# Optimization experiments

Measured on AMD Instinct MI355X. Metric: run time of the kernel, lower is better.

Reference implementation:

```python
import jax, jax.numpy as jnp
import numpy as np


def setup_inputs() -> dict:
    key = jax.random.key(0)
    ks = jax.random.split(key, 8)
    B, H, W, D, U = 128, 16, 48, 512, 512
    s = 1.0 / np.sqrt(D)
    return {
        "dec_hidden": jax.random.normal(ks[0], (B, D), jnp.float32),
        "enc_output": jax.random.normal(ks[1], (B, H, W, D), jnp.float32),
        "W1_w": jax.random.normal(ks[2], (D, U), jnp.float32) * s,
        "W1_b": jnp.zeros((U,), jnp.float32),
        "W2_w": jax.random.normal(ks[3], (D, U), jnp.float32) * s,
        "W2_b": jnp.zeros((U,), jnp.float32),
        "V_w": jax.random.normal(ks[4], (U, 1), jnp.float32) * (1.0 / np.sqrt(U)),
        "V_b": jnp.zeros((1,), jnp.float32),
    }


def reference(dec_hidden, enc_output, W1_w, W1_b, W2_w, W2_b, V_w, V_b):
    # dec_hidden: [B, Dd] -> [B, 1, 1, Dd]
    dec = dec_hidden[:, None, None, :]
    # W1(enc_output): [B, H, W, U]; W2(dec): [B, 1, 1, U] (broadcast add)
    h = jnp.tanh(jnp.einsum('bhwd,du->bhwu', enc_output, W1_w) + W1_b
                 + (dec @ W2_w + W2_b))
    # V(.) -> score [B, H, W, 1]
    score = jnp.einsum('bhwu,uo->bhwo', h, V_w) + V_b
    # softmax over axis=1 (H axis), matching tf.keras softmax(score, axis=1)
    attention_weights = jax.nn.softmax(score, axis=1)
    # context: sum over spatial axes -> [B, D]
    context_vector = jnp.sum(attention_weights * enc_output, axis=(1, 2))
    return context_vector, attention_weights
```

## Files before the change

### kernel.cpp

```cpp
#include <hip/hip_runtime.h>
#include <hip/hip_bf16.h>

typedef __attribute__((ext_vector_type(8))) short short8;
typedef __attribute__((ext_vector_type(4))) float f32x4;
typedef unsigned short ushort;

#define BB 128
#define HHH 16
#define WWW 48
#define DD 512
#define UU 512
#define ROWS_PER_B (HHH * WWW)
#define MTOT (BB * ROWS_PER_B)

__device__ __forceinline__ ushort f2bf(float f) {
    unsigned int u = __float_as_uint(f);
    u += 0x7fffu + ((u >> 16) & 1u);
    return (ushort)(u >> 16);
}

__device__ __forceinline__ void gload_lds16(const ushort* g, ushort* l) {
    __builtin_amdgcn_global_load_lds(
        (const __attribute__((address_space(1))) unsigned int*)(const void*)g,
        (__attribute__((address_space(3))) unsigned int*)(void*)l,
        16, 0, 0);
}

__global__ __launch_bounds__(256) void prep_kernel(
        const float* __restrict__ w1, const float* __restrict__ dec,
        const float* __restrict__ w2, const float* __restrict__ w1b,
        const float* __restrict__ w2b,
        ushort* __restrict__ w1p, float* __restrict__ dproj) {
    const int t = threadIdx.x;
    if (blockIdx.x < 64) {
        __shared__ __align__(16) ushort tile[64 * 72];
        const int u0 = (blockIdx.x & 7) * 64;
        const int kc = blockIdx.x >> 3;
        const int ul = t & 63;
        const int db = t >> 6;
#pragma unroll
        for (int i = 0; i < 16; ++i) {
            const int d = db + i * 4;
            tile[ul * 72 + d] = f2bf(w1[(size_t)(kc * 64 + d) * UU + u0 + ul]);
        }
        __syncthreads();
        const int u = t >> 2;
        const int s = (t & 3) * 2;
        const int x = u & 7;
        short8 v0 = *(const short8*)&tile[u * 72 + s * 8];
        short8 v1 = *(const short8*)&tile[u * 72 + s * 8 + 8];
        *(short8*)&w1p[(size_t)kc * 32768 + (u0 + u) * 64 + (( s      ^ x)) * 8] = v0;
        *(short8*)&w1p[(size_t)kc * 32768 + (u0 + u) * 64 + (((s + 1) ^ x)) * 8] = v1;
    } else {
        const int g = blockIdx.x - 64;
        const int b = g >> 1;
        const int u = (g & 1) * 256 + t;
        float acc = 0.f;
#pragma unroll 8
        for (int d = 0; d < DD; ++d)
            acc += dec[b * DD + d] * w2[(size_t)d * UU + u];
        dproj[b * UU + u] = acc + w1b[u] + w2b[u];
    }
}

__global__ __launch_bounds__(512, 2) void score_kernel(
        const float* __restrict__ enc, const ushort* __restrict__ w1p,
        const float* __restrict__ dproj, const float* __restrict__ vw,
        const float* __restrict__ vb, float* __restrict__ score) {
    __shared__ __align__(16) ushort Bb[2][UU * 64];
    __shared__ __align__(16) ushort Ab[2][128 * 64];

    const int tid  = threadIdx.x;
    const int lane = tid & 63;
    const int wave = tid >> 6;
    const int mbase = blockIdx.x * 128;
    const int b = mbase / ROWS_PER_B;

    const int mh   = wave >> 2;
    const int uc   = wave & 3;
    const int lrow = lane & 15;
    const int kgrp = lane >> 4;

    const int ar  = tid >> 2;
    const int asp = (tid & 3) * 2;
    const float* abase = enc + (size_t)(mbase + ar) * DD + asp * 8;
    const int s0p = ( asp      ^ (ar & 7)) * 8;
    const int s1p = ((asp + 1) ^ (ar & 7)) * 8;

    f32x4 acc[4][8] = {};

    {
        float4 a0 = ((const float4*)abase)[0];
        float4 a1 = ((const float4*)abase)[1];
        float4 a2 = ((const float4*)abase)[2];
        float4 a3 = ((const float4*)abase)[3];
        const ushort* bsrc = w1p + tid * 8;
#pragma unroll
        for (int i = 0; i < 8; ++i)
            gload_lds16(bsrc + i * 4096, &Bb[0][tid * 8 + i * 4096]);
        short8 w0, w1v;
        ushort* p0 = (ushort*)&w0; ushort* p1 = (ushort*)&w1v;
        p0[0]=f2bf(a0.x); p0[1]=f2bf(a0.y); p0[2]=f2bf(a0.z); p0[3]=f2bf(a0.w);
        p0[4]=f2bf(a1.x); p0[5]=f2bf(a1.y); p0[6]=f2bf(a1.z); p0[7]=f2bf(a1.w);
        p1[0]=f2bf(a2.x); p1[1]=f2bf(a2.y); p1[2]=f2bf(a2.z); p1[3]=f2bf(a2.w);
        p1[4]=f2bf(a3.x); p1[5]=f2bf(a3.y); p1[6]=f2bf(a3.z); p1[7]=f2bf(a3.w);
        *(short8*)&Ab[0][ar * 64 + s0p] = w0;
        *(short8*)&Ab[0][ar * 64 + s1p] = w1v;
    }

#pragma unroll
    for (int kc = 0; kc < 8; ++kc) {
        const int cur = kc & 1;
        __syncthreads();

        float4 a0, a1, a2, a3;
        if (kc < 7) {
            const float* asrc = abase + (kc + 1) * 64;
            a0 = ((const float4*)asrc)[0];
            a1 = ((const float4*)asrc)[1];
            a2 = ((const float4*)asrc)[2];
            a3 = ((const float4*)asrc)[3];
            const ushort* bsrc = w1p + (size_t)(kc + 1) * 32768 + tid * 8;
#pragma unroll
            for (int i = 0; i < 8; ++i)
                gload_lds16(bsrc + i * 4096, &Bb[cur ^ 1][tid * 8 + i * 4096]);
        }

        const ushort* Bc = &Bb[cur][0];
        const ushort* Ac = &Ab[cur][0];
#pragma unroll
        for (int kk = 0; kk < 2; ++kk) {
            const int sub = kk * 4 + kgrp;
            short8 afr[4], bfr[8];
#pragma unroll
            for (int ms = 0; ms < 4; ++ms) {
                const int r = mh * 64 + ms * 16 + lrow;
                afr[ms] = *(const short8*)&Ac[r * 64 + (sub ^ (r & 7)) * 8];
            }
#pragma unroll
            for (int uf = 0; uf < 8; ++uf) {
                const int u = uc * 128 + uf * 16 + lrow;
                bfr[uf] = *(const short8*)&Bc[u * 64 + (sub ^ (u & 7)) * 8];
            }
#pragma unroll
            for (int ms = 0; ms < 4; ++ms)
#pragma unroll
                for (int uf = 0; uf < 8; ++uf)
                    acc[ms][uf] = __builtin_amdgcn_mfma_f32_16x16x32_bf16(
                        afr[ms], bfr[uf], acc[ms][uf], 0, 0, 0);
        }

        if (kc < 7) {
            short8 w0, w1v;
            ushort* p0 = (ushort*)&w0; ushort* p1 = (ushort*)&w1v;
            p0[0]=f2bf(a0.x); p0[1]=f2bf(a0.y); p0[2]=f2bf(a0.z); p0[3]=f2bf(a0.w);
            p0[4]=f2bf(a1.x); p0[5]=f2bf(a1.y); p0[6]=f2bf(a1.z); p0[7]=f2bf(a1.w);
            p1[0]=f2bf(a2.x); p1[1]=f2bf(a2.y); p1[2]=f2bf(a2.z); p1[3]=f2bf(a2.w);
            p1[4]=f2bf(a3.x); p1[5]=f2bf(a3.y); p1[6]=f2bf(a3.z); p1[7]=f2bf(a3.w);
            *(short8*)&Ab[cur ^ 1][ar * 64 + s0p] = w0;
            *(short8*)&Ab[cur ^ 1][ar * 64 + s1p] = w1v;
        }
    }

    float part[4][4] = {};
#pragma unroll
    for (int uf = 0; uf < 8; ++uf) {
        const int u = uc * 128 + uf * 16 + lrow;
        const float cadd = dproj[b * UU + u];
        const float vwe  = vw[u];
#pragma unroll
        for (int ms = 0; ms < 4; ++ms)
#pragma unroll
            for (int j = 0; j < 4; ++j) {
                float x = acc[ms][uf][j] + cadd;
                x = fminf(fmaxf(x, -15.f), 15.f);
                float e = __expf(2.f * x);
                part[ms][j] += vwe * ((e - 1.f) / (e + 1.f));
            }
    }
#pragma unroll
    for (int off = 1; off < 16; off <<= 1)
#pragma unroll
        for (int ms = 0; ms < 4; ++ms)
#pragma unroll
            for (int j = 0; j < 4; ++j)
                part[ms][j] += __shfl_xor(part[ms][j], off, 64);

    float* scr = (float*)&Ab[0][0];
    if (lrow == 0) {
#pragma unroll
        for (int ms = 0; ms < 4; ++ms)
#pragma unroll
            for (int j = 0; j < 4; ++j)
                scr[uc * 128 + mh * 64 + ms * 16 + kgrp * 4 + j] = part[ms][j];
    }
    __syncthreads();
    if (tid < 128)
        score[mbase + tid] = scr[tid] + scr[128 + tid] + scr[256 + tid]
                           + scr[384 + tid] + vb[0];
}

__global__ __launch_bounds__(512) void ctx_kernel(
        const float* __restrict__ score, const float* __restrict__ enc,
        float* __restrict__ attn, float* __restrict__ partial) {
    __shared__ float sl[ROWS_PER_B];
    __shared__ float al[ROWS_PER_B];
    const int half = blockIdx.x;
    const int b    = blockIdx.y;
    const int t    = threadIdx.x;

    for (int i = t; i < ROWS_PER_B; i += 512) sl[i] = score[b * ROWS_PER_B + i];
    __syncthreads();

    if (t < WWW) {
        float v[HHH];
        float m = -1e30f;
#pragma unroll
        for (int h = 0; h < HHH; ++h) { v[h] = sl[h * WWW + t]; m = fmaxf(m, v[h]); }
        float sum = 0.f;
#pragma unroll
        for (int h = 0; h < HHH; ++h) { v[h] = __expf(v[h] - m); sum += v[h]; }
        const float inv = 1.f / sum;
#pragma unroll
        for (int h = 0; h < HHH; ++h) al[h * WWW + t] = v[h] * inv;
    }
    __syncthreads();

    const int rb = half * 384;
    for (int i = t; i < 384; i += 512)
        attn[b * ROWS_PER_B + rb + i] = al[rb + i];

    const int r0 = t >> 7;
    const int d4 = (t & 127) * 4;
    float4 acc = {0.f, 0.f, 0.f, 0.f};
    const float* ebase = enc + ((size_t)b * ROWS_PER_B + rb) * DD + d4;
#pragma unroll 8
    for (int i = 0; i < 96; ++i) {
        const int r = r0 + i * 4;
        const float a = al[rb + r];
        const float4 e = *(const float4*)(ebase + (size_t)r * DD);
        acc.x += a * e.x; acc.y += a * e.y; acc.z += a * e.z; acc.w += a * e.w;
    }
    *(float4*)(partial + ((size_t)((b * 2 + half) * 4 + r0)) * DD + d4) = acc;
}

__global__ void ctx_reduce_kernel(const float* __restrict__ partial,
                                  float* __restrict__ out) {
    const int q = blockIdx.x * 256 + threadIdx.x;
    const int b = q >> 7;
    const int d4 = (q & 127) * 4;
    float4 s = {0.f, 0.f, 0.f, 0.f};
#pragma unroll
    for (int j = 0; j < 8; ++j) {
        const float4 p = *(const float4*)(partial + ((size_t)(b * 8 + j)) * DD + d4);
        s.x += p.x; s.y += p.y; s.z += p.z; s.w += p.w;
    }
    *(float4*)(out + (size_t)b * DD + d4) = s;
}

extern "C" void kernel_launch(void* const* d_in, const int* in_sizes, int n_in,
                              void* d_out, int out_size, void* d_ws, size_t ws_size,
                              hipStream_t stream) {
    const float* dec = (const float*)d_in[0];
    const float* enc = (const float*)d_in[1];
    const float* w1w = (const float*)d_in[2];
    const float* w1b = (const float*)d_in[3];
    const float* w2w = (const float*)d_in[4];
    const float* w2b = (const float*)d_in[5];
    const float* vw  = (const float*)d_in[6];
    const float* vb  = (const float*)d_in[7];

    float* out = (float*)d_out;
    char* ws = (char*)d_ws;
    ushort* w1p    = (ushort*)(ws);
    float* dproj   = (float*)(ws + 524288);
    float* score   = (float*)(ws + 524288 + 262144);
    float* partial = (float*)(ws + 524288 + 262144 + 393216);

    float* ctx  = out;
    float* attn = out + BB * DD;

    prep_kernel<<<320, 256, 0, stream>>>(w1w, dec, w2w, w1b, w2b, w1p, dproj);
    score_kernel<<<MTOT / 128, 512, 0, stream>>>(enc, w1p, dproj, vw, vb, score);
    ctx_kernel<<<dim3(2, BB), 512, 0, stream>>>(score, enc, attn, partial);
    ctx_reduce_kernel<<<64, 256, 0, stream>>>(partial, ctx);
}
```

Before: 417.3 us.

## Split score GEMM over U halves with smaller tiles and single-buffered LDS

The score kernel now uses 64x256 tiles over a 2D grid that splits U into two halves. Each half writes a partial score, and the ctx kernel sums the two partials and adds the V bias. LDS double buffering is dropped for a simpler load-sync-compute-sync loop, which cuts shared memory per block so more blocks can be resident. The ctx kernel splits each batch into 4 row chunks instead of 2, and the bf16 conversion now uses plain round-half-up instead of round-to-nearest-even. In exchange, the enc A tile is loaded and converted twice (once per U half), and copy latency is no longer overlapped within a block.

Result: faster. 397.6 us (-4.7%).

```diff
diff --git a/kernel.cpp b/kernel.cpp
--- a/kernel.cpp
+++ b/kernel.cpp
@@ -12,11 +12,12 @@
 #define UU 512
 #define ROWS_PER_B (HHH * WWW)
 #define MTOT (BB * ROWS_PER_B)
+#define BM 64
+#define BN 256
+#define BK 64
 
 __device__ __forceinline__ ushort f2bf(float f) {
-    unsigned int u = __float_as_uint(f);
-    u += 0x7fffu + ((u >> 16) & 1u);
-    return (ushort)(u >> 16);
+    return (ushort)((__float_as_uint(f) + 0x8000u) >> 16);
 }
 
 __device__ __forceinline__ void gload_lds16(const ushort* g, ushort* l) {
@@ -63,109 +64,82 @@
     }
 }
 
-__global__ __launch_bounds__(512, 2) void score_kernel(
+__global__ __launch_bounds__(256, 4) void score_kernel(
         const float* __restrict__ enc, const ushort* __restrict__ w1p,
         const float* __restrict__ dproj, const float* __restrict__ vw,
-        const float* __restrict__ vb, float* __restrict__ score) {
-    __shared__ __align__(16) ushort Bb[2][UU * 64];
-    __shared__ __align__(16) ushort Ab[2][128 * 64];
+        float* __restrict__ scorep) {
+    __shared__ __align__(16) ushort Bb[BN * BK];
+    __shared__ __align__(16) ushort Ab[BM * BK];
 
     const int tid  = threadIdx.x;
     const int lane = tid & 63;
     const int wave = tid >> 6;
-    const int mbase = blockIdx.x * 128;
+    const int mbase = blockIdx.x * BM;
+    const int half  = blockIdx.y;
     const int b = mbase / ROWS_PER_B;
 
-    const int mh   = wave >> 2;
-    const int uc   = wave & 3;
     const int lrow = lane & 15;
     const int kgrp = lane >> 4;
 
     const int ar  = tid >> 2;
-    const int asp = (tid & 3) * 2;
-    const float* abase = enc + (size_t)(mbase + ar) * DD + asp * 8;
-    const int s0p = ( asp      ^ (ar & 7)) * 8;
-    const int s1p = ((asp + 1) ^ (ar & 7)) * 8;
-
-    f32x4 acc[4][8] = {};
-
-    {
-        float4 a0 = ((const float4*)abase)[0];
-        float4 a1 = ((const float4*)abase)[1];
-        float4 a2 = ((const float4*)abase)[2];
-        float4 a3 = ((const float4*)abase)[3];
-        const ushort* bsrc = w1p + tid * 8;
+    const int ac  = (tid & 3) * 2;
+    const float* abase = enc + (size_t)(mbase + ar) * DD + ac * 8;
+    const int s0p = ( ac      ^ (ar & 7)) * 8;
+    const int s1p = ((ac + 1) ^ (ar & 7)) * 8;
+    const ushort* bsrc0 = w1p + half * 16384 + tid * 8;
+
+    f32x4 acc[4][4] = {};
+
+    for (int kc = 0; kc < 8; ++kc) {
+        const ushort* bsrc = bsrc0 + (size_t)kc * 32768;
 #pragma unroll
         for (int i = 0; i < 8; ++i)
-            gload_lds16(bsrc + i * 4096, &Bb[0][tid * 8 + i * 4096]);
-        short8 w0, w1v;
-        ushort* p0 = (ushort*)&w0; ushort* p1 = (ushort*)&w1v;
-        p0[0]=f2bf(a0.x); p0[1]=f2bf(a0.y); p0[2]=f2bf(a0.z); p0[3]=f2bf(a0.w);
-        p0[4]=f2bf(a1.x); p0[5]=f2bf(a1.y); p0[6]=f2bf(a1.z); p0[7]=f2bf(a1.w);
-        p1[0]=f2bf(a2.x); p1[1]=f2bf(a2.y); p1[2]=f2bf(a2.z); p1[3]=f2bf(a2.w);
-        p1[4]=f2bf(a3.x); p1[5]=f2bf(a3.y); p1[6]=f2bf(a3.z); p1[7]=f2bf(a3.w);
-        *(short8*)&Ab[0][ar * 64 + s0p] = w0;
-        *(short8*)&Ab[0][ar * 64 + s1p] = w1v;
-    }
-
-#pragma unroll
-    for (int kc = 0; kc < 8; ++kc) {
-        const int cur = kc & 1;
-        __syncthreads();
-
-        float4 a0, a1, a2, a3;
-        if (kc < 7) {
-            const float* asrc = abase + (kc + 1) * 64;
-            a0 = ((const float4*)asrc)[0];
-            a1 = ((const float4*)asrc)[1];
-            a2 = ((const float4*)asrc)[2];
-            a3 = ((const float4*)asrc)[3];
-            const ushort* bsrc = w1p + (size_t)(kc + 1) * 32768 + tid * 8;
-#pragma unroll
-            for (int i = 0; i < 8; ++i)
-                gload_lds16(bsrc + i * 4096, &Bb[cur ^ 1][tid * 8 + i * 4096]);
-        }
-
-        const ushort* Bc = &Bb[cur][0];
-        const ushort* Ac = &Ab[cur][0];
-#pragma unroll
-        for (int kk = 0; kk < 2; ++kk) {
-            const int sub = kk * 4 + kgrp;
-            short8 afr[4], bfr[8];
-#pragma unroll
-            for (int ms = 0; ms < 4; ++ms) {
-                const int r = mh * 64 + ms * 16 + lrow;
-                afr[ms] = *(const short8*)&Ac[r * 64 + (sub ^ (r & 7)) * 8];
-            }
-#pragma unroll
-            for (int uf = 0; uf < 8; ++uf) {
-                const int u = uc * 128 + uf * 16 + lrow;
-                bfr[uf] = *(const short8*)&Bc[u * 64 + (sub ^ (u & 7)) * 8];
-            }
-#pragma unroll
-            for (int ms = 0; ms < 4; ++ms)
-#pragma unroll
-                for (int uf = 0; uf < 8; ++uf)
-                    acc[ms][uf] = __builtin_amdgcn_mfma_f32_16x16x32_bf16(
-                        afr[ms], bfr[uf], acc[ms][uf], 0, 0, 0);
-        }
-
-        if (kc < 7) {
+            gload_lds16(bsrc + i * 2048, &Bb[tid * 8 + i * 2048]);
+        {
+            const float* asrc = abase + kc * 64;
+            float4 a0 = ((const float4*)asrc)[0];
+            float4 a1 = ((const float4*)asrc)[1];
+            float4 a2 = ((const float4*)asrc)[2];
+            float4 a3 = ((const float4*)asrc)[3];
             short8 w0, w1v;
             ushort* p0 = (ushort*)&w0; ushort* p1 = (ushort*)&w1v;
             p0[0]=f2bf(a0.x); p0[1]=f2bf(a0.y); p0[2]=f2bf(a0.z); p0[3]=f2bf(a0.w);
             p0[4]=f2bf(a1.x); p0[5]=f2bf(a1.y); p0[6]=f2bf(a1.z); p0[7]=f2bf(a1.w);
             p1[0]=f2bf(a2.x); p1[1]=f2bf(a2.y); p1[2]=f2bf(a2.z); p1[3]=f2bf(a2.w);
             p1[4]=f2bf(a3.x); p1[5]=f2bf(a3.y); p1[6]=f2bf(a3.z); p1[7]=f2bf(a3.w);
-            *(short8*)&Ab[cur ^ 1][ar * 64 + s0p] = w0;
-            *(short8*)&Ab[cur ^ 1][ar * 64 + s1p] = w1v;
+            *(short8*)&Ab[ar * 64 + s0p] = w0;
+            *(short8*)&Ab[ar * 64 + s1p] = w1v;
         }
+        __syncthreads();
+
+#pragma unroll
+        for (int kk = 0; kk < 2; ++kk) {
+            const int sub = kk * 4 + kgrp;
+            short8 afr[4], bfr[4];
+#pragma unroll
+            for (int ms = 0; ms < 4; ++ms) {
+                const int r = ms * 16 + lrow;
+                afr[ms] = *(const short8*)&Ab[r * 64 + (sub ^ (r & 7)) * 8];
+            }
+#pragma unroll
+            for (int uf = 0; uf < 4; ++uf) {
+                const int u = wave * 64 + uf * 16 + lrow;
+                bfr[uf] = *(const short8*)&Bb[u * 64 + (sub ^ (u & 7)) * 8];
+            }
+#pragma unroll
+            for (int ms = 0; ms < 4; ++ms)
+#pragma unroll
+                for (int uf = 0; uf < 4; ++uf)
+                    acc[ms][uf] = __builtin_amdgcn_mfma_f32_16x16x32_bf16(
+                        afr[ms], bfr[uf], acc[ms][uf], 0, 0, 0);
+        }
+        __syncthreads();
     }
 
     float part[4][4] = {};
 #pragma unroll
-    for (int uf = 0; uf < 8; ++uf) {
-        const int u = uc * 128 + uf * 16 + lrow;
+    for (int uf = 0; uf < 4; ++uf) {
+        const int u = half * 256 + wave * 64 + uf * 16 + lrow;
         const float cadd = dproj[b * UU + u];
         const float vwe  = vw[u];
 #pragma unroll
@@ -186,30 +160,33 @@
             for (int j = 0; j < 4; ++j)
                 part[ms][j] += __shfl_xor(part[ms][j], off, 64);
 
-    float* scr = (float*)&Ab[0][0];
+    float* scr = (float*)&Ab[0];
     if (lrow == 0) {
 #pragma unroll
         for (int ms = 0; ms < 4; ++ms)
 #pragma unroll
             for (int j = 0; j < 4; ++j)
-                scr[uc * 128 + mh * 64 + ms * 16 + kgrp * 4 + j] = part[ms][j];
+                scr[wave * 64 + ms * 16 + kgrp * 4 + j] = part[ms][j];
     }
     __syncthreads();
-    if (tid < 128)
-        score[mbase + tid] = scr[tid] + scr[128 + tid] + scr[256 + tid]
-                           + scr[384 + tid] + vb[0];
+    if (tid < 64)
+        scorep[(size_t)half * MTOT + mbase + tid] =
+            scr[tid] + scr[64 + tid] + scr[128 + tid] + scr[192 + tid];
 }
 
 __global__ __launch_bounds__(512) void ctx_kernel(
-        const float* __restrict__ score, const float* __restrict__ enc,
+        const float* __restrict__ scorep, const float* __restrict__ enc,
+        const float* __restrict__ vb,
         float* __restrict__ attn, float* __restrict__ partial) {
     __shared__ float sl[ROWS_PER_B];
     __shared__ float al[ROWS_PER_B];
-    const int half = blockIdx.x;
-    const int b    = blockIdx.y;
-    const int t    = threadIdx.x;
-
-    for (int i = t; i < ROWS_PER_B; i += 512) sl[i] = score[b * ROWS_PER_B + i];
+    const int q = blockIdx.x;
+    const int b = blockIdx.y;
+    const int t = threadIdx.x;
+
+    const float vbv = vb[0];
+    for (int i = t; i < ROWS_PER_B; i += 512)
+        sl[i] = scorep[b * ROWS_PER_B + i] + scorep[MTOT + b * ROWS_PER_B + i] + vbv;
     __syncthreads();
 
     if (t < WWW) {
@@ -226,8 +203,8 @@
     }
     __syncthreads();
 
-    const int rb = half * 384;
-    for (int i = t; i < 384; i += 512)
+    const int rb = q * 192;
+    for (int i = t; i < 192; i += 512)
         attn[b * ROWS_PER_B + rb + i] = al[rb + i];
 
     const int r0 = t >> 7;
@@ -235,24 +212,24 @@
     float4 acc = {0.f, 0.f, 0.f, 0.f};
     const float* ebase = enc + ((size_t)b * ROWS_PER_B + rb) * DD + d4;
 #pragma unroll 8
-    for (int i = 0; i < 96; ++i) {
+    for (int i = 0; i < 48; ++i) {
         const int r = r0 + i * 4;
         const float a = al[rb + r];
         const float4 e = *(const float4*)(ebase + (size_t)r * DD);
         acc.x += a * e.x; acc.y += a * e.y; acc.z += a * e.z; acc.w += a * e.w;
     }
-    *(float4*)(partial + ((size_t)((b * 2 + half) * 4 + r0)) * DD + d4) = acc;
+    *(float4*)(partial + ((size_t)((b * 4 + q) * 4 + r0)) * DD + d4) = acc;
 }
 
 __global__ void ctx_reduce_kernel(const float* __restrict__ partial,
                                   float* __restrict__ out) {
-    const int q = blockIdx.x * 256 + threadIdx.x;
-    const int b = q >> 7;
-    const int d4 = (q & 127) * 4;
+    const int qd = blockIdx.x * 256 + threadIdx.x;
+    const int b = qd >> 7;
+    const int d4 = (qd & 127) * 4;
     float4 s = {0.f, 0.f, 0.f, 0.f};
 #pragma unroll
-    for (int j = 0; j < 8; ++j) {
-        const float4 p = *(const float4*)(partial + ((size_t)(b * 8 + j)) * DD + d4);
+    for (int j = 0; j < 16; ++j) {
+        const float4 p = *(const float4*)(partial + ((size_t)(b * 16 + j)) * DD + d4);
         s.x += p.x; s.y += p.y; s.z += p.z; s.w += p.w;
     }
     *(float4*)(out + (size_t)b * DD + d4) = s;
@@ -273,15 +250,15 @@
     float* out = (float*)d_out;
     char* ws = (char*)d_ws;
     ushort* w1p    = (ushort*)(ws);
-    float* dproj   = (float*)(ws + 524288);
-    float* score   = (float*)(ws + 524288 + 262144);
-    float* partial = (float*)(ws + 524288 + 262144 + 393216);
+    float* dproj   = (float*)(ws + (512 << 10));
+    float* scorep  = (float*)(ws + (768 << 10));
+    float* partial = (float*)(ws + (1536 << 10));
 
     float* ctx  = out;
     float* attn = out + BB * DD;
 
     prep_kernel<<<320, 256, 0, stream>>>(w1w, dec, w2w, w1b, w2b, w1p, dproj);
-    score_kernel<<<MTOT / 128, 512, 0, stream>>>(enc, w1p, dproj, vw, vb, score);
-    ctx_kernel<<<dim3(2, BB), 512, 0, stream>>>(score, enc, attn, partial);
+    score_kernel<<<dim3(MTOT / BM, 2), 256, 0, stream>>>(enc, w1p, dproj, vw, scorep);
+    ctx_kernel<<<dim3(4, BB), 512, 0, stream>>>(scorep, enc, vb, attn, partial);
     ctx_reduce_kernel<<<64, 256, 0, stream>>>(partial, ctx);
 }
```
